# Optimization experiments

Measured on AMD Instinct MI355X. Metric: run time of the kernel, lower is better.

The kernel has to match this reference:

```python
import jax, jax.numpy as jnp
import numpy as np

B, T, D, F, E, K = 2, 1024, 1024, 2048, 8, 2

def setup_inputs() -> dict:
    key = jax.random.key(0)
    ks = jax.random.split(key, 9)
    s = 0.02
    return {
        "states": jax.random.normal(ks[0], (B, T, D), dtype=jnp.float32),
        "Wg": jax.random.normal(ks[1], (D, E), dtype=jnp.float32) * s,
        "W_in": jax.random.normal(ks[2], (E, D, F), dtype=jnp.float32) * s,
        "b_in": jnp.zeros((E, F), dtype=jnp.float32),
        "W_scale": jax.random.normal(ks[3], (E, D, F), dtype=jnp.float32) * s,
        "b_scale": jnp.zeros((E, F), dtype=jnp.float32),
        "W_out": jax.random.normal(ks[4], (E, F, D), dtype=jnp.float32) * s,
        "b_out": jnp.zeros((E, D), dtype=jnp.float32),
        "num_selected": K,
    }

def reference(states, Wg, W_in, b_in, W_scale, b_scale, W_out, b_out, num_selected):
    b, t, d = states.shape
    x = states.reshape(-1, d)                      # [N, D]
    n = x.shape[0]
    # router: softmax over experts, then top-k + renormalize
    probs = jax.nn.softmax(x @ Wg, axis=-1)        # [N, E]
    topw, topi = jax.lax.top_k(probs, num_selected)  # [N, K]
    topw = topw / topw.sum(axis=-1, keepdims=True)
    # dense combine weights [N, E]: zero except selected experts
    w_full = jnp.zeros_like(probs).at[jnp.arange(n)[:, None], topi].set(topw)
    # gated-GELU expert MLPs, batched over experts
    h = jnp.einsum('nd,edf->enf', x, W_in) + b_in[:, None, :]       # [E, N, F]
    s = jnp.einsum('nd,edf->enf', x, W_scale) + b_scale[:, None, :]
    inner = jax.nn.gelu(h, approximate=False) * s                    # exact GELU (torch default)
    y = jnp.einsum('enf,efd->end', inner, W_out) + b_out[:, None, :]  # [E, N, D]
    out = jnp.einsum('end,ne->nd', y, w_full)                         # weighted combine
    return out.reshape(b, t, d)
```

## Files before the change

kernel.cpp:

```cpp
#include <hip/hip_runtime.h>
#include <hip/hip_bf16.h>
#include <math.h>

#define N_TOK 2048
#define DIM   1024
#define FF    2048
#define NEXP  8
#define NSLOT (N_TOK * 2)

typedef __attribute__((ext_vector_type(8))) short short8;
typedef __attribute__((ext_vector_type(4))) float f32x4;
typedef _Float16 half_t;
typedef __attribute__((ext_vector_type(4))) _Float16 h16x4;

__device__ __forceinline__ unsigned short f2bf(float f) {
    unsigned int u = __float_as_uint(f);
    u += 0x7FFFu + ((u >> 16) & 1u);
    return (unsigned short)(u >> 16);
}

#define GLOAD_LDS16(g, l) \
    __builtin_amdgcn_global_load_lds((const __attribute__((address_space(1))) unsigned int*)(g), \
                                     (__attribute__((address_space(3))) unsigned int*)(l), 16, 0, 0)

__global__ __launch_bounds__(256) void k_router(const float* __restrict__ x,
        const float* __restrict__ Wg, int* __restrict__ hdr,
        int* __restrict__ tok_e, float* __restrict__ tok_w) {
    int wave = threadIdx.x >> 6, lane = threadIdx.x & 63;
    int t = blockIdx.x * 4 + wave;
    float acc[NEXP];
#pragma unroll
    for (int e = 0; e < NEXP; ++e) acc[e] = 0.f;
    const float* xr = x + (size_t)t * DIM;
    for (int d = lane; d < DIM; d += 64) {
        float xv = xr[d];
        const float* wr = Wg + d * NEXP;
#pragma unroll
        for (int e = 0; e < NEXP; ++e) acc[e] += xv * wr[e];
    }
#pragma unroll
    for (int off = 32; off > 0; off >>= 1) {
#pragma unroll
        for (int e = 0; e < NEXP; ++e) acc[e] += __shfl_down(acc[e], off);
    }
    if (lane == 0) {
        int e0 = 0;
#pragma unroll
        for (int e = 1; e < NEXP; ++e) if (acc[e] > acc[e0]) e0 = e;
        int e1 = -1;
#pragma unroll
        for (int e = 0; e < NEXP; ++e) {
            if (e == e0) continue;
            if (e1 < 0 || acc[e] > acc[e1]) e1 = e;
        }
        float w0 = 1.f / (1.f + expf(acc[e1] - acc[e0]));
        tok_e[2 * t] = e0; tok_e[2 * t + 1] = e1;
        tok_w[2 * t] = w0; tok_w[2 * t + 1] = 1.f - w0;
        atomicAdd(&hdr[e0], 1);
        atomicAdd(&hdr[e1], 1);
    }
}

__global__ void k_scan(int* hdr) {
    if (threadIdx.x == 0 && blockIdx.x == 0) {
        int s = 0;
        for (int e = 0; e < NEXP; ++e) {
            hdr[16 + e] = s;
            hdr[8 + e]  = s;
            s += hdr[e];
        }
        hdr[24] = s;
    }
}

__global__ __launch_bounds__(256) void k_assign(const float* __restrict__ x,
        int* __restrict__ hdr, const int* __restrict__ tok_e,
        int* __restrict__ tok_slot, unsigned short* __restrict__ xg) {
    __shared__ int sh[2];
    int t = blockIdx.x;
    if (threadIdx.x == 0) {
        int e0 = tok_e[2 * t], e1 = tok_e[2 * t + 1];
        int p0 = atomicAdd(&hdr[8 + e0], 1);
        int p1 = atomicAdd(&hdr[8 + e1], 1);
        tok_slot[2 * t] = p0; tok_slot[2 * t + 1] = p1;
        sh[0] = p0; sh[1] = p1;
    }
    __syncthreads();
    int s0 = sh[0], s1 = sh[1];
    const float4* xr = (const float4*)(x + (size_t)t * DIM);
    float4 v = xr[threadIdx.x];
    ushort4 b;
    b.x = f2bf(v.x); b.y = f2bf(v.y); b.z = f2bf(v.z); b.w = f2bf(v.w);
    ((ushort4*)(xg + (size_t)s0 * DIM))[threadIdx.x] = b;
    ((ushort4*)(xg + (size_t)s1 * DIM))[threadIdx.x] = b;
}

__global__ __launch_bounds__(256) void k_cvt(const float* __restrict__ src,
        unsigned short* __restrict__ dst, int R, int C) {
    __shared__ unsigned short sh[64][65];
    const float* S = src + (size_t)blockIdx.z * R * C;
    unsigned short* Dp = dst + (size_t)blockIdx.z * R * C;
    int c0 = blockIdx.x * 64, r0 = blockIdx.y * 64;
    int t = threadIdx.x;
    int rr = t >> 2, c4 = (t & 3) * 4;
    const float* p = S + (size_t)(r0 + rr) * C + c0 + c4;
#pragma unroll
    for (int j = 0; j < 4; ++j) {
        float4 v = *(const float4*)(p + 16 * j);
        sh[rr][c4 + 16 * j + 0] = f2bf(v.x);
        sh[rr][c4 + 16 * j + 1] = f2bf(v.y);
        sh[rr][c4 + 16 * j + 2] = f2bf(v.z);
        sh[rr][c4 + 16 * j + 3] = f2bf(v.w);
    }
    __syncthreads();
    int oc = t >> 2, orr = (t & 3) * 16;
    unsigned short tmp[16];
#pragma unroll
    for (int j = 0; j < 16; ++j) tmp[j] = sh[orr + j][oc];
    unsigned short* q = Dp + (size_t)(c0 + oc) * R + r0 + orr;
    *(uint4*)q       = *(uint4*)&tmp[0];
    *(uint4*)(q + 8) = *(uint4*)&tmp[8];
}

__global__ __launch_bounds__(256, 4) void k_expert_hs(
        const unsigned short* __restrict__ xg,
        const unsigned short* __restrict__ Wth,
        const unsigned short* __restrict__ Wts,
        const float* __restrict__ b_in, const float* __restrict__ b_sc,
        const int* __restrict__ hdr, unsigned short* __restrict__ inner) {
    int e = blockIdx.z;
    int cnt = hdr[e];
    int mtile = blockIdx.y;
    if (mtile * 128 >= cnt) return;
    int base = hdr[16 + e];
    int f0 = blockIdx.x * 64;

    __shared__ unsigned short As[128 * 32];
    __shared__ unsigned short Bh[64 * 32];
    __shared__ unsigned short Bs[64 * 32];

    int tid = threadIdx.x;
    int wave = tid >> 6, lane = tid & 63;
    int lr = lane & 15, lq = lane >> 4;
    int wm = (wave >> 1) * 64, wf = (wave & 1) * 32;

    f32x4 acch[4][2], accs[4][2];
#pragma unroll
    for (int mi = 0; mi < 4; ++mi)
#pragma unroll
        for (int fi = 0; fi < 2; ++fi) {
            acch[mi][fi] = (f32x4){0.f, 0.f, 0.f, 0.f};
            accs[mi][fi] = (f32x4){0.f, 0.f, 0.f, 0.f};
        }

    int lrow = lane >> 2, lcol = (lane & 3) * 8;
    const unsigned short* Ab = xg  + (size_t)(base + mtile * 128 + wave * 16 + lrow) * DIM + lcol;
    const unsigned short* Hb = Wth + ((size_t)e * FF + f0 + wave * 16 + lrow) * DIM + lcol;
    const unsigned short* Sb = Wts + ((size_t)e * FF + f0 + wave * 16 + lrow) * DIM + lcol;

    for (int k0 = 0; k0 < DIM; k0 += 32) {
        __syncthreads();
        GLOAD_LDS16(Ab + k0, &As[(wave * 16) * 32]);
        GLOAD_LDS16(Ab + k0 + (size_t)64 * DIM, &As[(64 + wave * 16) * 32]);
        GLOAD_LDS16(Hb + k0, &Bh[(wave * 16) * 32]);
        GLOAD_LDS16(Sb + k0, &Bs[(wave * 16) * 32]);
        __syncthreads();

        short8 af[4], bhf[2], bsf[2];
#pragma unroll
        for (int mi = 0; mi < 4; ++mi)
            af[mi] = *(const short8*)&As[(wm + mi * 16 + lr) * 32 + lq * 8];
#pragma unroll
        for (int fi = 0; fi < 2; ++fi) {
            bhf[fi] = *(const short8*)&Bh[(wf + fi * 16 + lr) * 32 + lq * 8];
            bsf[fi] = *(const short8*)&Bs[(wf + fi * 16 + lr) * 32 + lq * 8];
        }
#pragma unroll
        for (int mi = 0; mi < 4; ++mi)
#pragma unroll
            for (int fi = 0; fi < 2; ++fi) {
                acch[mi][fi] = __builtin_amdgcn_mfma_f32_16x16x32_bf16(
                    af[mi], bhf[fi], acch[mi][fi], 0, 0, 0);
                accs[mi][fi] = __builtin_amdgcn_mfma_f32_16x16x32_bf16(
                    af[mi], bsf[fi], accs[mi][fi], 0, 0, 0);
            }
    }

#pragma unroll
    for (int fi = 0; fi < 2; ++fi) {
        int f = f0 + wf + fi * 16 + lr;
        float bi = b_in[e * FF + f];
        float bs2 = b_sc[e * FF + f];
#pragma unroll
        for (int mi = 0; mi < 4; ++mi) {
#pragma unroll
            for (int r = 0; r < 4; ++r) {
                int rl = wm + mi * 16 + lq * 4 + r;
                int grow = mtile * 128 + rl;
                if (grow < cnt) {
                    float h = acch[mi][fi][r] + bi;
                    float s = accs[mi][fi][r] + bs2;
                    float g = 0.5f * h * (1.f + erff(h * 0.70710678f));
                    inner[(size_t)(base + grow) * FF + f] = f2bf(g * s);
                }
            }
        }
    }
}

__global__ __launch_bounds__(256, 4) void k_expert_out(
        const unsigned short* __restrict__ inner,
        const unsigned short* __restrict__ Wto,
        const int* __restrict__ hdr, half_t* __restrict__ pbuf) {
    int e = blockIdx.z & 7;
    int ks = blockIdx.z >> 3;
    int cnt = hdr[e];
    int mtile = blockIdx.y;
    if (mtile * 128 >= cnt) return;
    int base = hdr[16 + e];
    int d0 = blockIdx.x * 128;

    __shared__ unsigned short As[128 * 32];
    __shared__ unsigned short Bt[128 * 32];

    int tid = threadIdx.x;
    int wave = tid >> 6, lane = tid & 63;
    int lr = lane & 15, lq = lane >> 4;
    int wm = (wave >> 1) * 64, wn = (wave & 1) * 64;

    f32x4 acc[4][4];
#pragma unroll
    for (int mi = 0; mi < 4; ++mi)
#pragma unroll
        for (int ni = 0; ni < 4; ++ni) acc[mi][ni] = (f32x4){0.f, 0.f, 0.f, 0.f};

    int lrow = lane >> 2, lcol = (lane & 3) * 8;
    const unsigned short* Ab = inner + (size_t)(base + mtile * 128 + wave * 16 + lrow) * FF + lcol;
    const unsigned short* Bb = Wto + ((size_t)e * DIM + d0 + wave * 16 + lrow) * FF + lcol;

    int kbeg = ks * (FF / 2), kend = kbeg + FF / 2;

    for (int k0 = kbeg; k0 < kend; k0 += 32) {
        __syncthreads();
        GLOAD_LDS16(Ab + k0, &As[(wave * 16) * 32]);
        GLOAD_LDS16(Ab + k0 + (size_t)64 * FF, &As[(64 + wave * 16) * 32]);
        GLOAD_LDS16(Bb + k0, &Bt[(wave * 16) * 32]);
        GLOAD_LDS16(Bb + k0 + (size_t)64 * FF, &Bt[(64 + wave * 16) * 32]);
        __syncthreads();

        short8 af[4], bfm[4];
#pragma unroll
        for (int mi = 0; mi < 4; ++mi)
            af[mi] = *(const short8*)&As[(wm + mi * 16 + lr) * 32 + lq * 8];
#pragma unroll
        for (int ni = 0; ni < 4; ++ni)
            bfm[ni] = *(const short8*)&Bt[(wn + ni * 16 + lr) * 32 + lq * 8];
#pragma unroll
        for (int mi = 0; mi < 4; ++mi)
#pragma unroll
            for (int ni = 0; ni < 4; ++ni)
                acc[mi][ni] = __builtin_amdgcn_mfma_f32_16x16x32_bf16(
                    af[mi], bfm[ni], acc[mi][ni], 0, 0, 0);
    }

    half_t* P = pbuf + (size_t)ks * NSLOT * DIM;
#pragma unroll
    for (int ni = 0; ni < 4; ++ni) {
        int d = d0 + wn + ni * 16 + lr;
#pragma unroll
        for (int mi = 0; mi < 4; ++mi) {
#pragma unroll
            for (int r = 0; r < 4; ++r) {
                int rl = wm + mi * 16 + lq * 4 + r;
                int grow = mtile * 128 + rl;
                if (grow < cnt)
                    P[(size_t)(base + grow) * DIM + d] = (half_t)acc[mi][ni][r];
            }
        }
    }
}

__global__ __launch_bounds__(256) void k_combine(const half_t* __restrict__ pbuf,
        const int* __restrict__ tok_slot, const int* __restrict__ tok_e,
        const float* __restrict__ tok_w, const float* __restrict__ b_out,
        float* __restrict__ out) {
    int t = blockIdx.x;
    int d = threadIdx.x * 4;
    int s0 = tok_slot[2 * t], s1 = tok_slot[2 * t + 1];
    int e0 = tok_e[2 * t], e1 = tok_e[2 * t + 1];
    float w0 = tok_w[2 * t], w1 = tok_w[2 * t + 1];
    const half_t* pA = pbuf;
    const half_t* pB = pbuf + (size_t)NSLOT * DIM;
    h16x4 a0 = *(const h16x4*)&pA[(size_t)s0 * DIM + d];
    h16x4 a1 = *(const h16x4*)&pB[(size_t)s0 * DIM + d];
    h16x4 c0 = *(const h16x4*)&pA[(size_t)s1 * DIM + d];
    h16x4 c1 = *(const h16x4*)&pB[(size_t)s1 * DIM + d];
    float4 b0 = *(const float4*)&b_out[e0 * DIM + d];
    float4 b1 = *(const float4*)&b_out[e1 * DIM + d];
    float4 r;
    r.x = w0 * ((float)a0.x + (float)a1.x + b0.x) + w1 * ((float)c0.x + (float)c1.x + b1.x);
    r.y = w0 * ((float)a0.y + (float)a1.y + b0.y) + w1 * ((float)c0.y + (float)c1.y + b1.y);
    r.z = w0 * ((float)a0.z + (float)a1.z + b0.z) + w1 * ((float)c0.z + (float)c1.z + b1.z);
    r.w = w0 * ((float)a0.w + (float)a1.w + b0.w) + w1 * ((float)c0.w + (float)c1.w + b1.w);
    *(float4*)&out[(size_t)t * DIM + d] = r;
}

extern "C" void kernel_launch(void* const* d_in, const int* in_sizes, int n_in,
                              void* d_out, int out_size, void* d_ws, size_t ws_size,
                              hipStream_t stream) {
    (void)in_sizes; (void)n_in; (void)out_size; (void)ws_size;
    const float* x    = (const float*)d_in[0];
    const float* Wg   = (const float*)d_in[1];
    const float* Win  = (const float*)d_in[2];
    const float* b_in = (const float*)d_in[3];
    const float* Wsc  = (const float*)d_in[4];
    const float* b_sc = (const float*)d_in[5];
    const float* Wout = (const float*)d_in[6];
    const float* b_out= (const float*)d_in[7];
    float* out = (float*)d_out;

    char* ws = (char*)d_ws;
    int*   hdr      = (int*)ws;
    int*   tok_e    = (int*)(ws + 256);
    float* tok_w    = (float*)(ws + 16640);
    int*   tok_slot = (int*)(ws + 33024);
    unsigned short* xg    = (unsigned short*)(ws + 65792);
    unsigned short* inner = (unsigned short*)(ws + 65792 + 8388608);
    half_t* pbuf = (half_t*)(ws + 65792 + 8388608 + 16777216);
    unsigned short* wt_h = (unsigned short*)(ws + 65792 + 8388608 + 16777216 + 16777216);
    unsigned short* wt_s = wt_h + (size_t)NEXP * FF * DIM;
    unsigned short* wt_o = wt_s + (size_t)NEXP * FF * DIM;

    hipMemsetAsync(hdr, 0, 256, stream);
    k_cvt<<<dim3(FF / 64, DIM / 64, NEXP), dim3(256), 0, stream>>>(Win,  wt_h, DIM, FF);
    k_cvt<<<dim3(FF / 64, DIM / 64, NEXP), dim3(256), 0, stream>>>(Wsc,  wt_s, DIM, FF);
    k_cvt<<<dim3(DIM / 64, FF / 64, NEXP), dim3(256), 0, stream>>>(Wout, wt_o, FF, DIM);
    k_router<<<dim3(N_TOK / 4), dim3(256), 0, stream>>>(x, Wg, hdr, tok_e, tok_w);
    k_scan<<<dim3(1), dim3(64), 0, stream>>>(hdr);
    k_assign<<<dim3(N_TOK), dim3(256), 0, stream>>>(x, hdr, tok_e, tok_slot, xg);
    k_expert_hs<<<dim3(FF / 64, 16, NEXP), dim3(256), 0, stream>>>(xg, wt_h, wt_s, b_in, b_sc, hdr, inner);
    k_expert_out<<<dim3(DIM / 128, 16, NEXP * 2), dim3(256), 0, stream>>>(inner, wt_o, hdr, pbuf);
    k_combine<<<dim3(N_TOK), dim3(256), 0, stream>>>(pbuf, tok_slot, tok_e, tok_w, b_out, out);
}
```

Measured before the change: 450.0 us.

## Enlarge expert GEMM tiles, swizzle LDS layout, merge weight conversion kernels

```diff
diff --git a/kernel.cpp b/kernel.cpp
--- a/kernel.cpp
+++ b/kernel.cpp
@@ -95,34 +95,42 @@
     ((ushort4*)(xg + (size_t)s1 * DIM))[threadIdx.x] = b;
 }
 
-__global__ __launch_bounds__(256) void k_cvt(const float* __restrict__ src,
-        unsigned short* __restrict__ dst, int R, int C) {
+__global__ __launch_bounds__(256) void k_cvt(
+        const float* __restrict__ s0, const float* __restrict__ s1,
+        const float* __restrict__ s2, unsigned short* __restrict__ d0,
+        unsigned short* __restrict__ d1, unsigned short* __restrict__ d2) {
+    int bz = blockIdx.y;
+    int which = bz >> 3, e = bz & 7;
+    int R = (which == 2) ? FF : DIM;
+    int C = (which == 2) ? DIM : FF;
+    const float* S = ((which == 0) ? s0 : (which == 1) ? s1 : s2) + (size_t)e * DIM * FF;
+    unsigned short* D = ((which == 0) ? d0 : (which == 1) ? d1 : d2) + (size_t)e * DIM * FF;
+    int tilesx = C >> 6;
+    int tx = blockIdx.x % tilesx, ty = blockIdx.x / tilesx;
+    int c0 = tx * 64, r0 = ty * 64;
     __shared__ unsigned short sh[64][65];
-    const float* S = src + (size_t)blockIdx.z * R * C;
-    unsigned short* Dp = dst + (size_t)blockIdx.z * R * C;
-    int c0 = blockIdx.x * 64, r0 = blockIdx.y * 64;
     int t = threadIdx.x;
-    int rr = t >> 2, c4 = (t & 3) * 4;
-    const float* p = S + (size_t)(r0 + rr) * C + c0 + c4;
+    int rr = t >> 4, cc = (t & 15) * 4;
 #pragma unroll
     for (int j = 0; j < 4; ++j) {
-        float4 v = *(const float4*)(p + 16 * j);
-        sh[rr][c4 + 16 * j + 0] = f2bf(v.x);
-        sh[rr][c4 + 16 * j + 1] = f2bf(v.y);
-        sh[rr][c4 + 16 * j + 2] = f2bf(v.z);
-        sh[rr][c4 + 16 * j + 3] = f2bf(v.w);
+        int r = rr + j * 16;
+        float4 v = *(const float4*)(S + (size_t)(r0 + r) * C + c0 + cc);
+        sh[r][cc + 0] = f2bf(v.x);
+        sh[r][cc + 1] = f2bf(v.y);
+        sh[r][cc + 2] = f2bf(v.z);
+        sh[r][cc + 3] = f2bf(v.w);
     }
     __syncthreads();
     int oc = t >> 2, orr = (t & 3) * 16;
     unsigned short tmp[16];
 #pragma unroll
     for (int j = 0; j < 16; ++j) tmp[j] = sh[orr + j][oc];
-    unsigned short* q = Dp + (size_t)(c0 + oc) * R + r0 + orr;
+    unsigned short* q = D + (size_t)(c0 + oc) * R + r0 + orr;
     *(uint4*)q       = *(uint4*)&tmp[0];
     *(uint4*)(q + 8) = *(uint4*)&tmp[8];
 }
 
-__global__ __launch_bounds__(256, 4) void k_expert_hs(
+__global__ __launch_bounds__(256, 2) void k_expert_hs(
         const unsigned short* __restrict__ xg,
         const unsigned short* __restrict__ Wth,
         const unsigned short* __restrict__ Wts,
@@ -133,52 +141,58 @@
     int mtile = blockIdx.y;
     if (mtile * 128 >= cnt) return;
     int base = hdr[16 + e];
-    int f0 = blockIdx.x * 64;
+    int f0 = blockIdx.x * 128;
 
     __shared__ unsigned short As[128 * 32];
-    __shared__ unsigned short Bh[64 * 32];
-    __shared__ unsigned short Bs[64 * 32];
+    __shared__ unsigned short Bh[128 * 32];
+    __shared__ unsigned short Bs[128 * 32];
 
     int tid = threadIdx.x;
     int wave = tid >> 6, lane = tid & 63;
     int lr = lane & 15, lq = lane >> 4;
-    int wm = (wave >> 1) * 64, wf = (wave & 1) * 32;
-
-    f32x4 acch[4][2], accs[4][2];
+    int wm = (wave >> 1) * 64, wf = (wave & 1) * 64;
+
+    f32x4 acch[4][4], accs[4][4];
 #pragma unroll
     for (int mi = 0; mi < 4; ++mi)
 #pragma unroll
-        for (int fi = 0; fi < 2; ++fi) {
+        for (int fi = 0; fi < 4; ++fi) {
             acch[mi][fi] = (f32x4){0.f, 0.f, 0.f, 0.f};
             accs[mi][fi] = (f32x4){0.f, 0.f, 0.f, 0.f};
         }
 
-    int lrow = lane >> 2, lcol = (lane & 3) * 8;
-    const unsigned short* Ab = xg  + (size_t)(base + mtile * 128 + wave * 16 + lrow) * DIM + lcol;
-    const unsigned short* Hb = Wth + ((size_t)e * FF + f0 + wave * 16 + lrow) * DIM + lcol;
-    const unsigned short* Sb = Wts + ((size_t)e * FF + f0 + wave * 16 + lrow) * DIM + lcol;
+    int swzc = (lane & 3) ^ ((lane >> 3) & 3);
+    int goff = (lane >> 2) * DIM + swzc * 8;
+    int rdo = lr * 32 + (lq ^ ((lr >> 1) & 3)) * 8;
+
+    const unsigned short* Abase = xg  + (size_t)(base + mtile * 128) * DIM + goff;
+    const unsigned short* Hbase = Wth + ((size_t)e * FF + f0) * DIM + goff;
+    const unsigned short* Sbase = Wts + ((size_t)e * FF + f0) * DIM + goff;
+    int p0 = wave * 32, p1 = wave * 32 + 16;
 
     for (int k0 = 0; k0 < DIM; k0 += 32) {
         __syncthreads();
-        GLOAD_LDS16(Ab + k0, &As[(wave * 16) * 32]);
-        GLOAD_LDS16(Ab + k0 + (size_t)64 * DIM, &As[(64 + wave * 16) * 32]);
-        GLOAD_LDS16(Hb + k0, &Bh[(wave * 16) * 32]);
-        GLOAD_LDS16(Sb + k0, &Bs[(wave * 16) * 32]);
+        GLOAD_LDS16(Abase + (size_t)p0 * DIM + k0, &As[p0 * 32]);
+        GLOAD_LDS16(Abase + (size_t)p1 * DIM + k0, &As[p1 * 32]);
+        GLOAD_LDS16(Hbase + (size_t)p0 * DIM + k0, &Bh[p0 * 32]);
+        GLOAD_LDS16(Hbase + (size_t)p1 * DIM + k0, &Bh[p1 * 32]);
+        GLOAD_LDS16(Sbase + (size_t)p0 * DIM + k0, &Bs[p0 * 32]);
+        GLOAD_LDS16(Sbase + (size_t)p1 * DIM + k0, &Bs[p1 * 32]);
         __syncthreads();
 
-        short8 af[4], bhf[2], bsf[2];
+        short8 af[4], bhf[4], bsf[4];
 #pragma unroll
         for (int mi = 0; mi < 4; ++mi)
-            af[mi] = *(const short8*)&As[(wm + mi * 16 + lr) * 32 + lq * 8];
-#pragma unroll
-        for (int fi = 0; fi < 2; ++fi) {
-            bhf[fi] = *(const short8*)&Bh[(wf + fi * 16 + lr) * 32 + lq * 8];
-            bsf[fi] = *(const short8*)&Bs[(wf + fi * 16 + lr) * 32 + lq * 8];
+            af[mi] = *(const short8*)&As[(wm + mi * 16) * 32 + rdo];
+#pragma unroll
+        for (int fi = 0; fi < 4; ++fi) {
+            bhf[fi] = *(const short8*)&Bh[(wf + fi * 16) * 32 + rdo];
+            bsf[fi] = *(const short8*)&Bs[(wf + fi * 16) * 32 + rdo];
         }
 #pragma unroll
         for (int mi = 0; mi < 4; ++mi)
 #pragma unroll
-            for (int fi = 0; fi < 2; ++fi) {
+            for (int fi = 0; fi < 4; ++fi) {
                 acch[mi][fi] = __builtin_amdgcn_mfma_f32_16x16x32_bf16(
                     af[mi], bhf[fi], acch[mi][fi], 0, 0, 0);
                 accs[mi][fi] = __builtin_amdgcn_mfma_f32_16x16x32_bf16(
@@ -187,7 +201,7 @@
     }
 
 #pragma unroll
-    for (int fi = 0; fi < 2; ++fi) {
+    for (int fi = 0; fi < 4; ++fi) {
         int f = f0 + wf + fi * 16 + lr;
         float bi = b_in[e * FF + f];
         float bs2 = b_sc[e * FF + f];
@@ -208,7 +222,7 @@
     }
 }
 
-__global__ __launch_bounds__(256, 4) void k_expert_out(
+__global__ __launch_bounds__(256, 2) void k_expert_out(
         const unsigned short* __restrict__ inner,
         const unsigned short* __restrict__ Wto,
         const int* __restrict__ hdr, half_t* __restrict__ pbuf) {
@@ -218,54 +232,60 @@
     int mtile = blockIdx.y;
     if (mtile * 128 >= cnt) return;
     int base = hdr[16 + e];
-    int d0 = blockIdx.x * 128;
+    int d0 = blockIdx.x * 256;
 
     __shared__ unsigned short As[128 * 32];
-    __shared__ unsigned short Bt[128 * 32];
+    __shared__ unsigned short Bt[256 * 32];
 
     int tid = threadIdx.x;
     int wave = tid >> 6, lane = tid & 63;
     int lr = lane & 15, lq = lane >> 4;
-    int wm = (wave >> 1) * 64, wn = (wave & 1) * 64;
-
-    f32x4 acc[4][4];
+    int wm = (wave >> 1) * 64, wn = (wave & 1) * 128;
+
+    f32x4 acc[4][8];
 #pragma unroll
     for (int mi = 0; mi < 4; ++mi)
 #pragma unroll
-        for (int ni = 0; ni < 4; ++ni) acc[mi][ni] = (f32x4){0.f, 0.f, 0.f, 0.f};
-
-    int lrow = lane >> 2, lcol = (lane & 3) * 8;
-    const unsigned short* Ab = inner + (size_t)(base + mtile * 128 + wave * 16 + lrow) * FF + lcol;
-    const unsigned short* Bb = Wto + ((size_t)e * DIM + d0 + wave * 16 + lrow) * FF + lcol;
+        for (int ni = 0; ni < 8; ++ni) acc[mi][ni] = (f32x4){0.f, 0.f, 0.f, 0.f};
+
+    int swzc = (lane & 3) ^ ((lane >> 3) & 3);
+    int goff = (lane >> 2) * FF + swzc * 8;
+    int rdo = lr * 32 + (lq ^ ((lr >> 1) & 3)) * 8;
+
+    const unsigned short* Abase = inner + (size_t)(base + mtile * 128) * FF + goff;
+    const unsigned short* Bbase = Wto + ((size_t)e * DIM + d0) * FF + goff;
+    int pa0 = wave * 32, pa1 = wave * 32 + 16;
+    int pb0 = wave * 64;
 
     int kbeg = ks * (FF / 2), kend = kbeg + FF / 2;
 
     for (int k0 = kbeg; k0 < kend; k0 += 32) {
         __syncthreads();
-        GLOAD_LDS16(Ab + k0, &As[(wave * 16) * 32]);
-        GLOAD_LDS16(Ab + k0 + (size_t)64 * FF, &As[(64 + wave * 16) * 32]);
-        GLOAD_LDS16(Bb + k0, &Bt[(wave * 16) * 32]);
-        GLOAD_LDS16(Bb + k0 + (size_t)64 * FF, &Bt[(64 + wave * 16) * 32]);
+        GLOAD_LDS16(Abase + (size_t)pa0 * FF + k0, &As[pa0 * 32]);
+        GLOAD_LDS16(Abase + (size_t)pa1 * FF + k0, &As[pa1 * 32]);
+#pragma unroll
+        for (int j = 0; j < 4; ++j)
+            GLOAD_LDS16(Bbase + (size_t)(pb0 + j * 16) * FF + k0, &Bt[(pb0 + j * 16) * 32]);
         __syncthreads();
 
-        short8 af[4], bfm[4];
+        short8 af[4], bfm[8];
 #pragma unroll
         for (int mi = 0; mi < 4; ++mi)
-            af[mi] = *(const short8*)&As[(wm + mi * 16 + lr) * 32 + lq * 8];
-#pragma unroll
-        for (int ni = 0; ni < 4; ++ni)
-            bfm[ni] = *(const short8*)&Bt[(wn + ni * 16 + lr) * 32 + lq * 8];
+            af[mi] = *(const short8*)&As[(wm + mi * 16) * 32 + rdo];
+#pragma unroll
+        for (int ni = 0; ni < 8; ++ni)
+            bfm[ni] = *(const short8*)&Bt[(wn + ni * 16) * 32 + rdo];
 #pragma unroll
         for (int mi = 0; mi < 4; ++mi)
 #pragma unroll
-            for (int ni = 0; ni < 4; ++ni)
+            for (int ni = 0; ni < 8; ++ni)
                 acc[mi][ni] = __builtin_amdgcn_mfma_f32_16x16x32_bf16(
                     af[mi], bfm[ni], acc[mi][ni], 0, 0, 0);
     }
 
     half_t* P = pbuf + (size_t)ks * NSLOT * DIM;
 #pragma unroll
-    for (int ni = 0; ni < 4; ++ni) {
+    for (int ni = 0; ni < 8; ++ni) {
         int d = d0 + wn + ni * 16 + lr;
 #pragma unroll
         for (int mi = 0; mi < 4; ++mi) {
@@ -332,13 +352,11 @@
     unsigned short* wt_o = wt_s + (size_t)NEXP * FF * DIM;
 
     hipMemsetAsync(hdr, 0, 256, stream);
-    k_cvt<<<dim3(FF / 64, DIM / 64, NEXP), dim3(256), 0, stream>>>(Win,  wt_h, DIM, FF);
-    k_cvt<<<dim3(FF / 64, DIM / 64, NEXP), dim3(256), 0, stream>>>(Wsc,  wt_s, DIM, FF);
-    k_cvt<<<dim3(DIM / 64, FF / 64, NEXP), dim3(256), 0, stream>>>(Wout, wt_o, FF, DIM);
+    k_cvt<<<dim3(512, 24), dim3(256), 0, stream>>>(Win, Wsc, Wout, wt_h, wt_s, wt_o);
     k_router<<<dim3(N_TOK / 4), dim3(256), 0, stream>>>(x, Wg, hdr, tok_e, tok_w);
     k_scan<<<dim3(1), dim3(64), 0, stream>>>(hdr);
     k_assign<<<dim3(N_TOK), dim3(256), 0, stream>>>(x, hdr, tok_e, tok_slot, xg);
-    k_expert_hs<<<dim3(FF / 64, 16, NEXP), dim3(256), 0, stream>>>(xg, wt_h, wt_s, b_in, b_sc, hdr, inner);
-    k_expert_out<<<dim3(DIM / 128, 16, NEXP * 2), dim3(256), 0, stream>>>(inner, wt_o, hdr, pbuf);
+    k_expert_hs<<<dim3(FF / 128, 16, NEXP), dim3(256), 0, stream>>>(xg, wt_h, wt_s, b_in, b_sc, hdr, inner);
+    k_expert_out<<<dim3(DIM / 256, 16, NEXP * 2), dim3(256), 0, stream>>>(inner, wt_o, hdr, pbuf);
     k_combine<<<dim3(N_TOK), dim3(256), 0, stream>>>(pbuf, tok_slot, tok_e, tok_w, b_out, out);
 }
```

After: 457.3 us. About the same (+1.6%).
